# Optimization experiments

Hardware: AMD Instinct MI355X
Metric: run time of the kernel (lower is better)

The kernel has to match this reference:

```python
import jax, jax.numpy as jnp
import numpy as np


def setup_inputs() -> dict:
    key = jax.random.key(0)
    k1, k2 = jax.random.split(key)
    B, C, T, H, W = 4, 256, 8, 32, 32
    K = 1024  # num_embeddings
    z = jax.random.normal(k1, (B, C, T, H, W), dtype=jnp.float32)
    # original init: uniform(-1/K, 1/K)
    emb_weight = jax.random.uniform(k2, (K, C), dtype=jnp.float32,
                                    minval=-1.0 / K, maxval=1.0 / K)
    return {"z": z, "emb_weight": emb_weight}


def reference(z, emb_weight):
    B, C, T, H, W = z.shape
    # (B,C,T,H,W) -> (N, C) with N = B*T*H*W
    z_flat = jnp.transpose(z, (0, 2, 3, 4, 1)).reshape(-1, C)
    # squared L2 distances via ||a||^2 + ||b||^2 - 2 a.b  (fused, vectorized;
    # no python batching loop needed)
    d = (jnp.sum(z_flat * z_flat, axis=1, keepdims=True)
         + jnp.sum(emb_weight * emb_weight, axis=1)
         - 2.0 * z_flat @ emb_weight.T)  # (N, K)
    indices = jnp.argmin(d, axis=1)  # (N,)
    z_q = emb_weight[indices]  # (N, C) gather
    z_q = jnp.transpose(z_q.reshape(B, T, H, W, C), (0, 4, 1, 2, 3))
    # straight-through estimator
    z_q = z + jax.lax.stop_gradient(z_q - z)
    return z_q, indices.reshape(B, T, H, W)
```

## Files before the change

kernel.cpp:

```cpp
#include <hip/hip_runtime.h>
#include <hip/hip_bf16.h>


#define DEVI __device__ __forceinline__

typedef __attribute__((ext_vector_type(8))) short bf16x8;
typedef __attribute__((ext_vector_type(4))) float f32x4;

#define C_DIM   256
#define K_CODES 1024
#define S_DIM   8192
#define N_ROWS  32768
#define ZQ_ELEMS 8388608
#define TILE_M  64
#define NCHUNK  32
#define BAND1   1.0e-3f
#define REC_CAP 8192
#define UCAP    832
#define FLT_BIG 3.402823466e+38f

#define WS_EFR  0
#define WS_E2F  524288
#define WS_CNT  528384
#define WS_REC  528448

DEVI unsigned short f2b(float f) {
    unsigned u = __float_as_uint(f);
    u += 0x7FFFu + ((u >> 16) & 1u);
    return (unsigned short)(u >> 16);
}
DEVI unsigned umin2(unsigned a, unsigned b) { return a < b ? a : b; }
DEVI unsigned umax2(unsigned a, unsigned b) { return a > b ? a : b; }
DEVI unsigned long long ullmin2(unsigned long long a, unsigned long long b) {
    return a < b ? a : b;
}

DEVI f32x4 MF(bf16x8 a, bf16x8 b, f32x4 c) {
    return __builtin_amdgcn_mfma_f32_16x16x32_bf16(a, b, c, 0, 0, 0);
}
DEVI bf16x8 ldsfrag(const char* L, int row, int coff) {
    const int byte = row * 512 + (coff ^ ((row & 7) << 4));
    return *reinterpret_cast<const bf16x8*>(L + byte);
}

__global__ void vq_prep(const float* __restrict__ E,
                        unsigned short* __restrict__ efrag,
                        float* __restrict__ e2f, int* __restrict__ gcnt) {
    const int k = blockIdx.x;
    const int lane = threadIdx.x;
    if (k == 0 && lane == 0) *gcnt = 0;
    const float4 v = reinterpret_cast<const float4*>(E + (size_t)k * C_DIM)[lane];
    double s = (double)v.x * v.x + (double)v.y * v.y
             + (double)v.z * v.z + (double)v.w * v.w;
    ushort4 h;
    h.x = f2b(v.x); h.y = f2b(v.y); h.z = f2b(v.z); h.w = f2b(v.w);
    const int f = lane >> 1, half = lane & 1;
    const int ks = f >> 2, q = f & 3;
    const int jj = k & 15, wn = (k >> 4) & 1, chunk = k >> 5;
    char* dst = (char*)efrag + (size_t)chunk * 16384 + wn * 8192
              + ks * 1024 + (q * 16 + jj) * 16 + half * 8;
    *reinterpret_cast<ushort4*>(dst) = h;
#pragma unroll
    for (int m = 32; m; m >>= 1) s += __shfl_xor(s, m, 64);
    if (lane == 0) e2f[k] = (float)s;
}

__global__ __launch_bounds__(256, 2) void vq_main(
        const float* __restrict__ z, const float* __restrict__ E,
        const unsigned short* __restrict__ efrag,
        const float* __restrict__ e2f,
        float* __restrict__ out_zq, float* __restrict__ out_idx,
        int* __restrict__ gcnt, int2* __restrict__ grec) {
    __shared__ __align__(16) char smraw[65792];
    __shared__ float e2p[1024];
    __shared__ int   kfinA[64];
    __shared__ int   flagA[64];
    __shared__ float znS[64];
    __shared__ unsigned long long best64[64];
    __shared__ int   units[UCAP];
    __shared__ int   ucnt;

    const int tid = threadIdx.x;
    const int n0 = blockIdx.x * TILE_M;
    const int b  = n0 >> 13;
    const int s0 = n0 & (S_DIM - 1);

    {
        const float4 v = reinterpret_cast<const float4*>(e2f)[tid];
        float4 w; w.x = 1.0f + v.x; w.y = 1.0f + v.y;
        w.z = 1.0f + v.z; w.w = 1.0f + v.w;
        reinterpret_cast<float4*>(e2p)[tid] = w;
    }

    {
        const int s  = tid & 63;
        const int cg = tid >> 6;
        const float* zb = z + (size_t)b * (C_DIM * S_DIM) + s0 + s;
#pragma unroll
        for (int ci = 0; ci < 16; ++ci) {
            const int c = cg * 4 + ci * 16;
            ushort4 h;
            h.x = f2b(zb[(size_t)(c + 0) * S_DIM]);
            h.y = f2b(zb[(size_t)(c + 1) * S_DIM]);
            h.z = f2b(zb[(size_t)(c + 2) * S_DIM]);
            h.w = f2b(zb[(size_t)(c + 3) * S_DIM]);
            const int byte = s * 512 + ((c * 2) ^ ((s & 7) << 4));
            *reinterpret_cast<ushort4*>(smraw + byte) = h;
        }
    }
    __syncthreads();

    const int w    = tid >> 6;
    const int lane = tid & 63;
    const int wm   = w >> 1, wn = w & 1;
    const int q    = lane >> 4, jj = lane & 15;
    const int mycol = wn * 16 + jj;

    bf16x8 Ah0[8], Ah1[8];
    {
        const int r0 = wm * 32 + jj, r1 = r0 + 16;
#pragma unroll
        for (int ks = 0; ks < 8; ++ks) {
            const int coff = ks * 64 + q * 16;
            Ah0[ks] = ldsfrag(smraw, r0, coff);
            Ah1[ks] = ldsfrag(smraw, r1, coff);
        }
    }

    const char* gB = (const char*)efrag + (size_t)wn * 8192 + (size_t)lane * 16;

#define LOADB(BR, N)                                                          \
    { _Pragma("unroll")                                                       \
      for (int ks_ = 0; ks_ < 8; ++ks_)                                       \
          BR[ks_] = *reinterpret_cast<const bf16x8*>(                         \
              gB + (size_t)(N) * 16384 + ks_ * 1024); }

#define RCOMPUTE(BR, A0, A1)                                                  \
    { A0 = (f32x4){0.f, 0.f, 0.f, 0.f}; A1 = A0;                              \
      _Pragma("unroll")                                                       \
      for (int ks_ = 0; ks_ < 8; ++ks_) {                                     \
          A0 = MF(Ah0[ks_], BR[ks_], A0);                                     \
          A1 = MF(Ah1[ks_], BR[ks_], A1);                                     \
      } }

#define UPD(A0, A1, E2V, N)                                                   \
    { _Pragma("unroll")                                                       \
      for (int r = 0; r < 4; ++r) {                                           \
          unsigned t_ = (__float_as_uint(                                     \
              __builtin_fmaf(-2.f, A0[r], E2V)) & 0xFFFFFFE0u) | (unsigned)(N);\
          unsigned lo_ = umin2(K1[r], t_), hi_ = umax2(K1[r], t_);            \
          K1[r] = lo_; K2[r] = umin2(K2[r], hi_);                             \
          t_ = (__float_as_uint(                                              \
              __builtin_fmaf(-2.f, A1[r], E2V)) & 0xFFFFFFE0u) | (unsigned)(N);\
          lo_ = umin2(K1[4 + r], t_); hi_ = umax2(K1[4 + r], t_);             \
          K1[4 + r] = lo_; K2[4 + r] = umin2(K2[4 + r], hi_);                 \
      } }

    unsigned K1[8], K2[8];
#pragma unroll
    for (int i = 0; i < 8; ++i) { K1[i] = 0xFFFFFFFFu; K2[i] = 0xFFFFFFFFu; }

    bf16x8 Bc[8], Bn[8];
    LOADB(Bc, 0)
    LOADB(Bn, 1)
    f32x4 aA0, aA1, aB0, aB1;

#pragma unroll
    for (int p = 0; p < 16; ++p) {
        const int nA = 2 * p, nB = 2 * p + 1;
        RCOMPUTE(Bc, aA0, aA1)
        if (p < 15) LOADB(Bc, nA + 2)
        UPD(aA0, aA1, e2p[nA * 32 + mycol], nA)
        RCOMPUTE(Bn, aB0, aB1)
        if (p < 15) LOADB(Bn, nB + 2)
        UPD(aB0, aB1, e2p[nB * 32 + mycol], nB)
    }

    __syncthreads();
    if (tid == 0) ucnt = 0;
    for (int i = tid; i < UCAP; i += 256) units[i] = -1;
#pragma unroll
    for (int t = 0; t < 2; ++t) {
#pragma unroll
        for (int r = 0; r < 4; ++r) {
            const int sl = t * 4 + r;
            const int row = wm * 32 + t * 16 + q * 4 + r;
            *reinterpret_cast<int2*>(smraw + row * 272 + mycol * 8) =
                make_int2((int)K1[sl], (int)K2[sl]);
        }
    }
    __syncthreads();

    if (tid < 64) {
        const char* dmp = smraw + tid * 272;
        unsigned kmin = 0xFFFFFFFFu; int emin = 0;
#pragma unroll 4
        for (int e = 0; e < 32; ++e) {
            const unsigned k1 = (unsigned)
                reinterpret_cast<const int2*>(dmp + e * 8)->x;
            if (k1 < kmin) { kmin = k1; emin = e; }
        }
        const int kmincode = (int)((kmin & 31u) << 5) | emin;
        const float dminf = __uint_as_float(kmin & 0xFFFFFFE0u);
        const unsigned limk =
            (__float_as_uint(dminf + BAND1) & 0xFFFFFFE0u) | 31u;
        int cnt = 0, nfb = 0, fb0 = 0, fb1 = 0;
#pragma unroll 4
        for (int e = 0; e < 32; ++e) {
            const int2 v = *reinterpret_cast<const int2*>(dmp + e * 8);
            if ((unsigned)v.x <= limk) {
                const int code = (int)(((unsigned)v.x & 31u) << 5) | e;
                cnt += (code != kmincode);
            }
            if ((unsigned)v.y <= limk) {
                if (nfb == 0) fb0 = e; else if (nfb == 1) fb1 = e;
                ++nfb;
            }
        }
        kfinA[tid] = kmincode;
        flagA[tid] = 0;
        if (cnt > 0 || nfb > 0) {
            bool ov = (cnt > 16 || nfb > 2);
            if (!ov) {
                const int need = 1 + cnt + 32 * nfb;
                const int base = atomicAdd(&ucnt, need);
                if (base + need <= UCAP) {
                    flagA[tid] = 1;
                    best64[tid] = 0xFFFFFFFFFFFFFFFFull;
                    int p = base;
                    units[p++] = (tid << 10) | kmincode;
                    for (int e = 0; e < 32; ++e) {
                        const int2 v = *reinterpret_cast<const int2*>(dmp + e * 8);
                        if ((unsigned)v.x <= limk) {
                            const int code = (int)(((unsigned)v.x & 31u) << 5) | e;
                            if (code != kmincode) units[p++] = (tid << 10) | code;
                        }
                    }
                    if (nfb >= 1)
                        for (int c = 0; c < 32; ++c)
                            units[p++] = (tid << 10) | (c << 5) | fb0;
                    if (nfb >= 2)
                        for (int c = 0; c < 32; ++c)
                            units[p++] = (tid << 10) | (c << 5) | fb1;
                } else ov = true;
            }
            if (ov) {
                const int slot = atomicAdd(gcnt, 1);
                if (slot < REC_CAP) grec[slot] = make_int2(n0 + tid, kmincode);
            }
        }
    }
    __syncthreads();

    {
        const int s  = tid & 63;
        const int cg = tid >> 6;
        const float* zb = z + (size_t)b * (C_DIM * S_DIM) + s0 + s;
        float* zr = reinterpret_cast<float*>(smraw) + s * 257;
#pragma unroll
        for (int ci = 0; ci < 16; ++ci) {
            const int c = cg * 4 + ci * 16;
            zr[c + 0] = zb[(size_t)(c + 0) * S_DIM];
            zr[c + 1] = zb[(size_t)(c + 1) * S_DIM];
            zr[c + 2] = zb[(size_t)(c + 2) * S_DIM];
            zr[c + 3] = zb[(size_t)(c + 3) * S_DIM];
        }
    }
    __syncthreads();

    if (tid < 64 && flagA[tid]) {
        const float* zr = reinterpret_cast<const float*>(smraw) + tid * 257;
        double a0 = 0.0, a1 = 0.0, a2 = 0.0, a3 = 0.0;
#pragma unroll 8
        for (int c = 0; c < 256; c += 4) {
            const double v0 = zr[c], v1 = zr[c+1], v2 = zr[c+2], v3 = zr[c+3];
            a0 = fma(v0, v0, a0); a1 = fma(v1, v1, a1);
            a2 = fma(v2, v2, a2); a3 = fma(v3, v3, a3);
        }
        znS[tid] = (float)((a0 + a1) + (a2 + a3));
    }
    __syncthreads();

    {
        const int nu = (ucnt < UCAP) ? ucnt : UCAP;
        for (int u = tid; u < nu; u += 256) {
            const int enc = units[u];
            if (enc < 0) continue;
            const int row = enc >> 10, k = enc & 1023;
            const float* zr = reinterpret_cast<const float*>(smraw) + row * 257;
            const float* er = E + (size_t)k * C_DIM;
            double a0 = 0.0, a1 = 0.0, a2 = 0.0, a3 = 0.0;
#pragma unroll 8
            for (int c = 0; c < 256; c += 4) {
                a0 = fma((double)zr[c+0], (double)er[c+0], a0);
                a1 = fma((double)zr[c+1], (double)er[c+1], a1);
                a2 = fma((double)zr[c+2], (double)er[c+2], a2);
                a3 = fma((double)zr[c+3], (double)er[c+3], a3);
            }
            const float t32 = (float)((a0 + a1) + (a2 + a3));
            const float d = (znS[row] + e2f[k]) - 2.0f * t32;
            const unsigned long long key =
                ((unsigned long long)__float_as_uint(d) << 32) | (unsigned)k;
            atomicMin(&best64[row], key);
        }
    }
    __syncthreads();

    if (tid < 64) {
        if (flagA[tid])
            kfinA[tid] = (int)(best64[tid] & 0xFFFFFFFFull);
        out_idx[n0 + tid] = (float)kfinA[tid];
    }

#pragma unroll
    for (int h = 0; h < 2; ++h) {
        __syncthreads();
        {
            const int slot = tid & 31;
            const int cg   = tid >> 5;
            const int kk   = kfinA[h * 32 + slot];
            const float4* er = reinterpret_cast<const float4*>(
                E + (size_t)kk * C_DIM + cg * 32);
            float* lb = reinterpret_cast<float*>(smraw) + slot * 257 + cg * 32;
#pragma unroll
            for (int i = 0; i < 8; ++i) {
                const float4 v = er[i];
                lb[4 * i + 0] = v.x; lb[4 * i + 1] = v.y;
                lb[4 * i + 2] = v.z; lb[4 * i + 3] = v.w;
            }
        }
        __syncthreads();
        {
            const int sg = tid & 31;
            const int cg = tid >> 5;
            float* ob = out_zq + (size_t)b * (C_DIM * S_DIM) + s0 + h * 32 + sg;
            const float* lr = reinterpret_cast<const float*>(smraw) + sg * 257;
#pragma unroll
            for (int i = 0; i < 32; ++i) {
                const int c = cg * 32 + i;
                ob[(size_t)c * S_DIM] = lr[c];
            }
        }
    }
}

__global__ __launch_bounds__(256) void vq_fall(
        const float* __restrict__ z, const float* __restrict__ E,
        const float* __restrict__ e2f,
        const int* __restrict__ gcnt, const int2* __restrict__ grec,
        float* __restrict__ out_zq, float* __restrict__ out_idx) {
    __shared__ float zsh[256];
    __shared__ double dpart[4];
    __shared__ unsigned long long wbest[4];

    const int tid = threadIdx.x;
    const int w = tid >> 6, lane = tid & 63;
    int count = gcnt[0]; if (count > REC_CAP) count = REC_CAP;

    for (int ri = blockIdx.x; ri < count; ri += gridDim.x) {
        const int2 rc = grec[ri];
        const int n = rc.x, kmin = rc.y;
        const int b = n >> 13, s = n & (S_DIM - 1);
        __syncthreads();
        const float zc = z[((size_t)(b * C_DIM + tid)) * S_DIM + s];
        zsh[tid] = zc;
        double p = (double)zc * (double)zc;
#pragma unroll
        for (int m = 32; m; m >>= 1) p += __shfl_xor(p, m, 64);
        if (lane == 0) dpart[w] = p;
        __syncthreads();
        const float znf = (float)((dpart[0] + dpart[1]) + (dpart[2] + dpart[3]));

        unsigned long long best = 0xFFFFFFFFFFFFFFFFull;
        for (int j = 0; j < 4; ++j) {
            const int k = j * 256 + tid;
            const float4* er = reinterpret_cast<const float4*>(
                E + (size_t)k * C_DIM);
            double a0 = 0.0, a1 = 0.0, a2 = 0.0, a3 = 0.0;
#pragma unroll 8
            for (int i = 0; i < 64; ++i) {
                const float4 ev = er[i];
                const float4 zl = reinterpret_cast<const float4*>(zsh)[i];
                a0 = fma((double)zl.x, (double)ev.x, a0);
                a1 = fma((double)zl.y, (double)ev.y, a1);
                a2 = fma((double)zl.z, (double)ev.z, a2);
                a3 = fma((double)zl.w, (double)ev.w, a3);
            }
            const float t32 = (float)((a0 + a1) + (a2 + a3));
            const float d = (znf + e2f[k]) - 2.0f * t32;
            best = ullmin2(best,
                ((unsigned long long)__float_as_uint(d) << 32) | (unsigned)k);
        }
#pragma unroll
        for (int m = 32; m; m >>= 1)
            best = ullmin2(best, (unsigned long long)__shfl_xor(
                (long long)best, m, 64));
        if (lane == 0) wbest[w] = best;
        __syncthreads();
        const unsigned long long fin =
            ullmin2(ullmin2(wbest[0], wbest[1]), ullmin2(wbest[2], wbest[3]));
        const int bk = (int)(fin & 0xFFFFFFFFull);
        if (tid == 0) out_idx[n] = (float)bk;
        if (bk != kmin) {
            out_zq[((size_t)(b * C_DIM + tid)) * S_DIM + s] =
                E[(size_t)bk * C_DIM + tid];
        }
    }
}

extern "C" void kernel_launch(void* const* d_in, const int* in_sizes, int n_in,
                              void* d_out, int out_size, void* d_ws, size_t ws_size,
                              hipStream_t stream) {
    (void)in_sizes; (void)n_in; (void)out_size; (void)ws_size;
    const float* z = (const float*)d_in[0];
    const float* E = (const float*)d_in[1];
    char* wsb = (char*)d_ws;
    unsigned short* efrag = (unsigned short*)(wsb + WS_EFR);
    float* e2f = (float*)(wsb + WS_E2F);
    int*   cnt = (int*)  (wsb + WS_CNT);
    int2*  rec = (int2*) (wsb + WS_REC);
    float* out = (float*)d_out;

    vq_prep<<<dim3(K_CODES), dim3(64), 0, stream>>>(E, efrag, e2f, cnt);
    vq_main<<<dim3(N_ROWS / TILE_M), dim3(256), 0, stream>>>(
        z, E, efrag, e2f, out, out + ZQ_ELEMS, cnt, rec);
    vq_fall<<<dim3(1024), dim3(256), 0, stream>>>(
        z, E, e2f, cnt, rec, out, out + ZQ_ELEMS);
}
```

Baseline: 55.29 us.

## Halve row tile to 32 rows per block and raise occupancy to 4 blocks/CU

Shrinks the main kernel's row tile from 64 to 32 rows, so each wave keeps one A fragment set and one accumulator instead of two. LDS use and register arrays shrink to match, and launch bounds now request 4 blocks per CU. The goal is more resident waves and more blocks in flight to hide global memory latency. In exchange, each streamed codebook chunk is reused by half as many rows, which doubles total codebook fragment traffic and makes the MFMA work per load lighter.

```diff
diff --git a/kernel.cpp b/kernel.cpp
--- a/kernel.cpp
+++ b/kernel.cpp
@@ -12,11 +12,11 @@
 #define S_DIM   8192
 #define N_ROWS  32768
 #define ZQ_ELEMS 8388608
-#define TILE_M  64
+#define TILE_M  32
 #define NCHUNK  32
 #define BAND1   1.0e-3f
 #define REC_CAP 8192
-#define UCAP    832
+#define UCAP    416
 #define FLT_BIG 3.402823466e+38f
 
 #define WS_EFR  0
@@ -65,18 +65,18 @@
     if (lane == 0) e2f[k] = (float)s;
 }
 
-__global__ __launch_bounds__(256, 2) void vq_main(
+__global__ __launch_bounds__(256, 4) void vq_main(
         const float* __restrict__ z, const float* __restrict__ E,
         const unsigned short* __restrict__ efrag,
         const float* __restrict__ e2f,
         float* __restrict__ out_zq, float* __restrict__ out_idx,
         int* __restrict__ gcnt, int2* __restrict__ grec) {
-    __shared__ __align__(16) char smraw[65792];
+    __shared__ __align__(16) char smraw[32896];
     __shared__ float e2p[1024];
-    __shared__ int   kfinA[64];
-    __shared__ int   flagA[64];
-    __shared__ float znS[64];
-    __shared__ unsigned long long best64[64];
+    __shared__ int   kfinA[32];
+    __shared__ int   flagA[32];
+    __shared__ float znS[32];
+    __shared__ unsigned long long best64[32];
     __shared__ int   units[UCAP];
     __shared__ int   ucnt;
 
@@ -93,12 +93,12 @@
     }
 
     {
-        const int s  = tid & 63;
-        const int cg = tid >> 6;
+        const int s  = tid & 31;
+        const int cg = tid >> 5;
         const float* zb = z + (size_t)b * (C_DIM * S_DIM) + s0 + s;
 #pragma unroll
-        for (int ci = 0; ci < 16; ++ci) {
-            const int c = cg * 4 + ci * 16;
+        for (int ci = 0; ci < 8; ++ci) {
+            const int c = cg * 4 + ci * 32;
             ushort4 h;
             h.x = f2b(zb[(size_t)(c + 0) * S_DIM]);
             h.y = f2b(zb[(size_t)(c + 1) * S_DIM]);
@@ -116,15 +116,12 @@
     const int q    = lane >> 4, jj = lane & 15;
     const int mycol = wn * 16 + jj;
 
-    bf16x8 Ah0[8], Ah1[8];
-    {
-        const int r0 = wm * 32 + jj, r1 = r0 + 16;
-#pragma unroll
-        for (int ks = 0; ks < 8; ++ks) {
-            const int coff = ks * 64 + q * 16;
-            Ah0[ks] = ldsfrag(smraw, r0, coff);
-            Ah1[ks] = ldsfrag(smraw, r1, coff);
-        }
+    bf16x8 Ah[8];
+    {
+        const int r0 = wm * 16 + jj;
+#pragma unroll
+        for (int ks = 0; ks < 8; ++ks)
+            Ah[ks] = ldsfrag(smraw, r0, ks * 64 + q * 16);
     }
 
     const char* gB = (const char*)efrag + (size_t)wn * 8192 + (size_t)lane * 16;
@@ -135,63 +132,52 @@
           BR[ks_] = *reinterpret_cast<const bf16x8*>(                         \
               gB + (size_t)(N) * 16384 + ks_ * 1024); }
 
-#define RCOMPUTE(BR, A0, A1)                                                  \
-    { A0 = (f32x4){0.f, 0.f, 0.f, 0.f}; A1 = A0;                              \
+#define RCOMPUTE(BR, A0)                                                      \
+    { A0 = (f32x4){0.f, 0.f, 0.f, 0.f};                                       \
       _Pragma("unroll")                                                       \
-      for (int ks_ = 0; ks_ < 8; ++ks_) {                                     \
-          A0 = MF(Ah0[ks_], BR[ks_], A0);                                     \
-          A1 = MF(Ah1[ks_], BR[ks_], A1);                                     \
-      } }
-
-#define UPD(A0, A1, E2V, N)                                                   \
+      for (int ks_ = 0; ks_ < 8; ++ks_) A0 = MF(Ah[ks_], BR[ks_], A0); }
+
+#define UPD(A0, E2V, N)                                                       \
     { _Pragma("unroll")                                                       \
       for (int r = 0; r < 4; ++r) {                                           \
-          unsigned t_ = (__float_as_uint(                                     \
+          const unsigned t_ = (__float_as_uint(                               \
               __builtin_fmaf(-2.f, A0[r], E2V)) & 0xFFFFFFE0u) | (unsigned)(N);\
-          unsigned lo_ = umin2(K1[r], t_), hi_ = umax2(K1[r], t_);            \
+          const unsigned lo_ = umin2(K1[r], t_), hi_ = umax2(K1[r], t_);      \
           K1[r] = lo_; K2[r] = umin2(K2[r], hi_);                             \
-          t_ = (__float_as_uint(                                              \
-              __builtin_fmaf(-2.f, A1[r], E2V)) & 0xFFFFFFE0u) | (unsigned)(N);\
-          lo_ = umin2(K1[4 + r], t_); hi_ = umax2(K1[4 + r], t_);             \
-          K1[4 + r] = lo_; K2[4 + r] = umin2(K2[4 + r], hi_);                 \
       } }
 
-    unsigned K1[8], K2[8];
-#pragma unroll
-    for (int i = 0; i < 8; ++i) { K1[i] = 0xFFFFFFFFu; K2[i] = 0xFFFFFFFFu; }
+    unsigned K1[4], K2[4];
+#pragma unroll
+    for (int i = 0; i < 4; ++i) { K1[i] = 0xFFFFFFFFu; K2[i] = 0xFFFFFFFFu; }
 
     bf16x8 Bc[8], Bn[8];
     LOADB(Bc, 0)
     LOADB(Bn, 1)
-    f32x4 aA0, aA1, aB0, aB1;
+    f32x4 aA, aB;
 
 #pragma unroll
     for (int p = 0; p < 16; ++p) {
         const int nA = 2 * p, nB = 2 * p + 1;
-        RCOMPUTE(Bc, aA0, aA1)
+        RCOMPUTE(Bc, aA)
         if (p < 15) LOADB(Bc, nA + 2)
-        UPD(aA0, aA1, e2p[nA * 32 + mycol], nA)
-        RCOMPUTE(Bn, aB0, aB1)
+        UPD(aA, e2p[nA * 32 + mycol], nA)
+        RCOMPUTE(Bn, aB)
         if (p < 15) LOADB(Bn, nB + 2)
-        UPD(aB0, aB1, e2p[nB * 32 + mycol], nB)
+        UPD(aB, e2p[nB * 32 + mycol], nB)
     }
 
     __syncthreads();
     if (tid == 0) ucnt = 0;
     for (int i = tid; i < UCAP; i += 256) units[i] = -1;
 #pragma unroll
-    for (int t = 0; t < 2; ++t) {
-#pragma unroll
-        for (int r = 0; r < 4; ++r) {
-            const int sl = t * 4 + r;
-            const int row = wm * 32 + t * 16 + q * 4 + r;
-            *reinterpret_cast<int2*>(smraw + row * 272 + mycol * 8) =
-                make_int2((int)K1[sl], (int)K2[sl]);
-        }
-    }
-    __syncthreads();
-
-    if (tid < 64) {
+    for (int r = 0; r < 4; ++r) {
+        const int row = wm * 16 + q * 4 + r;
+        *reinterpret_cast<int2*>(smraw + row * 272 + mycol * 8) =
+            make_int2((int)K1[r], (int)K2[r]);
+    }
+    __syncthreads();
+
+    if (tid < 32) {
         const char* dmp = smraw + tid * 272;
         unsigned kmin = 0xFFFFFFFFu; int emin = 0;
 #pragma unroll 4
@@ -253,13 +239,13 @@
     __syncthreads();
 
     {
-        const int s  = tid & 63;
-        const int cg = tid >> 6;
+        const int s  = tid & 31;
+        const int cg = tid >> 5;
         const float* zb = z + (size_t)b * (C_DIM * S_DIM) + s0 + s;
         float* zr = reinterpret_cast<float*>(smraw) + s * 257;
 #pragma unroll
-        for (int ci = 0; ci < 16; ++ci) {
-            const int c = cg * 4 + ci * 16;
+        for (int ci = 0; ci < 8; ++ci) {
+            const int c = cg * 4 + ci * 32;
             zr[c + 0] = zb[(size_t)(c + 0) * S_DIM];
             zr[c + 1] = zb[(size_t)(c + 1) * S_DIM];
             zr[c + 2] = zb[(size_t)(c + 2) * S_DIM];
@@ -268,7 +254,7 @@
     }
     __syncthreads();
 
-    if (tid < 64 && flagA[tid]) {
+    if (tid < 32 && flagA[tid]) {
         const float* zr = reinterpret_cast<const float*>(smraw) + tid * 257;
         double a0 = 0.0, a1 = 0.0, a2 = 0.0, a3 = 0.0;
 #pragma unroll 8
@@ -306,40 +292,37 @@
     }
     __syncthreads();
 
-    if (tid < 64) {
+    if (tid < 32) {
         if (flagA[tid])
             kfinA[tid] = (int)(best64[tid] & 0xFFFFFFFFull);
         out_idx[n0 + tid] = (float)kfinA[tid];
     }
-
-#pragma unroll
-    for (int h = 0; h < 2; ++h) {
-        __syncthreads();
-        {
-            const int slot = tid & 31;
-            const int cg   = tid >> 5;
-            const int kk   = kfinA[h * 32 + slot];
-            const float4* er = reinterpret_cast<const float4*>(
-                E + (size_t)kk * C_DIM + cg * 32);
-            float* lb = reinterpret_cast<float*>(smraw) + slot * 257 + cg * 32;
-#pragma unroll
-            for (int i = 0; i < 8; ++i) {
-                const float4 v = er[i];
-                lb[4 * i + 0] = v.x; lb[4 * i + 1] = v.y;
-                lb[4 * i + 2] = v.z; lb[4 * i + 3] = v.w;
-            }
-        }
-        __syncthreads();
-        {
-            const int sg = tid & 31;
-            const int cg = tid >> 5;
-            float* ob = out_zq + (size_t)b * (C_DIM * S_DIM) + s0 + h * 32 + sg;
-            const float* lr = reinterpret_cast<const float*>(smraw) + sg * 257;
-#pragma unroll
-            for (int i = 0; i < 32; ++i) {
-                const int c = cg * 32 + i;
-                ob[(size_t)c * S_DIM] = lr[c];
-            }
+    __syncthreads();
+
+    {
+        const int slot = tid & 31;
+        const int cg   = tid >> 5;
+        const int kk   = kfinA[slot];
+        const float4* er = reinterpret_cast<const float4*>(
+            E + (size_t)kk * C_DIM + cg * 32);
+        float* lb = reinterpret_cast<float*>(smraw) + slot * 257 + cg * 32;
+#pragma unroll
+        for (int i = 0; i < 8; ++i) {
+            const float4 v = er[i];
+            lb[4 * i + 0] = v.x; lb[4 * i + 1] = v.y;
+            lb[4 * i + 2] = v.z; lb[4 * i + 3] = v.w;
+        }
+    }
+    __syncthreads();
+    {
+        const int sg = tid & 31;
+        const int cg = tid >> 5;
+        float* ob = out_zq + (size_t)b * (C_DIM * S_DIM) + s0 + sg;
+        const float* lr = reinterpret_cast<const float*>(smraw) + sg * 257;
+#pragma unroll
+        for (int i = 0; i < 32; ++i) {
+            const int c = cg * 32 + i;
+            ob[(size_t)c * S_DIM] = lr[c];
         }
     }
 }
```

Result: slower. 70.04 us (+26.7%).
